# Kernel optimization log

Measured on AMD Instinct MI355X. Metric: run time of the kernel, lower is better.

The kernel has to match this reference:

```python
import jax, jax.numpy as jnp
import numpy as np

COMMITMENT_COST = 0.25
B, T, D = 32, 2048, 64
K = 1024


def setup_inputs() -> dict:
    key = jax.random.key(0)
    k1, k2 = jax.random.split(key)
    inputs = jax.random.normal(k1, (B, T, D), dtype=jnp.float32)
    # codebook init: uniform(-1/K, 1/K) in the original; use same scale
    embedding = jax.random.uniform(k2, (K, D), dtype=jnp.float32,
                                   minval=-1.0 / K, maxval=1.0 / K)
    return {"inputs": inputs, "embedding": embedding}


def reference(inputs, embedding):
    Bb, Tt, Dd = inputs.shape
    flat = inputs.reshape(-1, Dd)  # [N, D]
    dist = (jnp.sum(flat * flat, axis=1, keepdims=True)
            + jnp.sum(embedding * embedding, axis=1)[None, :]
            - 2.0 * (flat @ embedding.T))
    encoding_indices = jnp.argmin(dist, axis=1)  # [N]
    quantized = embedding[encoding_indices].reshape(Bb, Tt, Dd)
    # commitment loss: mse(stop_grad(quantized), inputs)
    e_latent_loss = jnp.mean((jax.lax.stop_gradient(quantized) - inputs) ** 2)
    vq_loss = COMMITMENT_COST * e_latent_loss
    codebook_loss = jnp.zeros((), dtype=jnp.float32)
    # straight-through estimator
    quantized_st = inputs + jax.lax.stop_gradient(quantized - inputs)
    return (quantized_st, encoding_indices.reshape(Bb, Tt),
            vq_loss, e_latent_loss, codebook_loss)
```

## Files before the change

### kernel.cpp

```cpp
#include <hip/hip_runtime.h>
#include <hip/hip_bf16.h>
#include <math.h>


typedef __attribute__((ext_vector_type(8))) short bf16x8;
typedef __attribute__((ext_vector_type(4))) float f32x4;

namespace {
constexpr int NROWS  = 65536;
constexpr int DDIM   = 64;
constexpr int KCODES = 1024;
constexpr float EPSB = 4e-5f;

constexpr size_t WS_LOSS = 0;
constexpr size_t WS_CNT  = 64;
constexpr size_t WS_SE   = 256;
constexpr size_t WS_EHB  = 8192;
constexpr size_t WS_ELB  = WS_EHB + (size_t)65536 * 2;
constexpr size_t WS_BIDX = WS_ELB + (size_t)65536 * 2;
constexpr size_t WS_LIST = WS_BIDX + (size_t)NROWS * 4;
constexpr size_t WS_KEY  = WS_LIST + (size_t)NROWS * 4;
constexpr size_t WS_MV   = WS_KEY + (size_t)NROWS * 8;
constexpr size_t WS_KV   = WS_MV + (size_t)4 * NROWS * 8;
}

__device__ inline short f2bf(float v) {
  __hip_bfloat16 h = __float2bfloat16(v);
  return *reinterpret_cast<short*>(&h);
}
__device__ inline float bf2f(short s) {
  __hip_bfloat16 h;
  *reinterpret_cast<short*>(&h) = s;
  return __bfloat162float(h);
}
__device__ inline f32x4 mfma16(bf16x8 a, bf16x8 b, f32x4 c) {
  return __builtin_amdgcn_mfma_f32_16x16x32_bf16(a, b, c, 0, 0, 0);
}
__device__ inline unsigned int fflip(unsigned int b) {
  return b ^ ((unsigned int)((int)b >> 31) | 0x80000000u);
}

__global__ __launch_bounds__(256) void vq_prep(const float* __restrict__ emb,
                                               float* __restrict__ se,
                                               short* __restrict__ ehB,
                                               short* __restrict__ elB,
                                               unsigned long long* __restrict__ keyBest,
                                               double* __restrict__ loss_accum,
                                               int* __restrict__ cnt) {
  #pragma clang fp contract(off)
  const int gid = blockIdx.x * 256 + (int)threadIdx.x;
  if (gid == 0) { *loss_accum = 0.0; *cnt = 0; }
  keyBest[gid] = ~0ull;

  if (gid < KCODES) {
    const float* e = emb + (size_t)gid * DDIM;
    float r[8];
    #pragma unroll
    for (int j = 0; j < 8; ++j) r[j] = e[j] * e[j];
    #pragma unroll
    for (int i = 8; i < DDIM; i += 8) {
      #pragma unroll
      for (int j = 0; j < 8; ++j) r[j] += e[i + j] * e[i + j];
    }
    se[gid] = ((r[0] + r[1]) + (r[2] + r[3])) + ((r[4] + r[5]) + (r[6] + r[7]));
  }

  if (gid < 8192) {
    const int t  = gid >> 7;
    const int dc = (gid >> 6) & 1;
    const int l  = gid & 63;
    const int code = t * 16 + (l & 15);
    const int d0   = dc * 32 + (l >> 4) * 8;
    const float* ep = emb + (size_t)code * DDIM + d0;
    const size_t ob = ((size_t)(t * 2 + dc) * 64 + l) * 8;
    #pragma unroll
    for (int i = 0; i < 8; ++i) {
      const float v = ep[i];
      const short h = f2bf(v);
      ehB[ob + i] = h;
      elB[ob + i] = f2bf(v - bf2f(h));
    }
  }
}

__global__ __launch_bounds__(256, 2) void vq_fused(const float* __restrict__ x,
                                                   const short* __restrict__ ehB,
                                                   const short* __restrict__ elB,
                                                   const float* __restrict__ se,
                                                   float2* __restrict__ mv,
                                                   unsigned long long* __restrict__ kv) {
  #pragma clang fp contract(off)
  __shared__ float sel[256];
  const int tid  = (int)threadIdx.x;
  const int l    = tid & 63;
  const int wid  = tid >> 6;
  const int quar = (int)blockIdx.x & 3;
  const int rblk = (int)blockIdx.x >> 2;
  const int t0   = quar * 16;
  sel[tid] = se[t0 * 16 + tid];
  __syncthreads();

  const int wrb = rblk * 128 + wid * 32;
  bf16x8 xh[2][2], xl[2][2];
  #pragma unroll
  for (int rt = 0; rt < 2; ++rt) {
    const float* xp = x + (size_t)(wrb + rt * 16 + (l & 15)) * DDIM + (l >> 4) * 8;
    #pragma unroll
    for (int dc = 0; dc < 2; ++dc) {
      const float4 v0 = *reinterpret_cast<const float4*>(xp + dc * 32);
      const float4 v1 = *reinterpret_cast<const float4*>(xp + dc * 32 + 4);
      const float vv[8] = {v0.x, v0.y, v0.z, v0.w, v1.x, v1.y, v1.z, v1.w};
      #pragma unroll
      for (int i = 0; i < 8; ++i) {
        const short h = f2bf(vv[i]);
        xh[rt][dc][i] = h;
        xl[rt][dc][i] = f2bf(vv[i] - bf2f(h));
      }
    }
  }

  float m1v[2][4], m2v[2][4];
  int   m1t[2][4];
  #pragma unroll
  for (int rt = 0; rt < 2; ++rt)
    #pragma unroll
    for (int r = 0; r < 4; ++r) { m1v[rt][r] = INFINITY; m2v[rt][r] = INFINITY; m1t[rt][r] = 0; }

  const size_t lb = (size_t)l * 8;
#define FRAGLD(buf, tt, half2) \
  (*reinterpret_cast<const bf16x8*>((buf) + (size_t)(tt) * 1024 + (half2) * 512 + lb))

  bf16x8 c0 = FRAGLD(ehB, t0, 0), c1 = FRAGLD(ehB, t0, 1),
         c2 = FRAGLD(elB, t0, 0), c3 = FRAGLD(elB, t0, 1);
  bf16x8 n0 = FRAGLD(ehB, t0 + 1, 0), n1 = FRAGLD(ehB, t0 + 1, 1),
         n2 = FRAGLD(elB, t0 + 1, 0), n3 = FRAGLD(elB, t0 + 1, 1);

  const f32x4 kz = {0.f, 0.f, 0.f, 0.f};
  #pragma unroll 4
  for (int tt = 0; tt < 16; ++tt) {
    const int t = t0 + tt;
    const int tf = (tt + 2 < 16) ? t + 2 : t0 + 15;
    bf16x8 f0 = FRAGLD(ehB, tf, 0), f1 = FRAGLD(ehB, tf, 1),
           f2 = FRAGLD(elB, tf, 0), f3 = FRAGLD(elB, tf, 1);

    f32x4 a0, a1;
    a0 = mfma16(xh[0][0], c0, kz);  a1 = mfma16(xh[1][0], c0, kz);
    a0 = mfma16(xh[0][1], c1, a0);  a1 = mfma16(xh[1][1], c1, a1);
    a0 = mfma16(xh[0][0], c2, a0);  a1 = mfma16(xh[1][0], c2, a1);
    a0 = mfma16(xh[0][1], c3, a0);  a1 = mfma16(xh[1][1], c3, a1);
    a0 = mfma16(xl[0][0], c0, a0);  a1 = mfma16(xl[1][0], c0, a1);
    a0 = mfma16(xl[0][1], c1, a0);  a1 = mfma16(xl[1][1], c1, a1);

    const float sev = sel[tt * 16 + (l & 15)];
    #pragma unroll
    for (int r = 0; r < 4; ++r) {
      {
        const float d = __builtin_fmaf(-2.0f, a0[r], sev);
        const bool c = d < m1v[0][r];
        m2v[0][r] = fminf(m2v[0][r], fmaxf(m1v[0][r], d));
        m1t[0][r] = c ? t : m1t[0][r];
        m1v[0][r] = fminf(m1v[0][r], d);
      }
      {
        const float d = __builtin_fmaf(-2.0f, a1[r], sev);
        const bool c = d < m1v[1][r];
        m2v[1][r] = fminf(m2v[1][r], fmaxf(m1v[1][r], d));
        m1t[1][r] = c ? t : m1t[1][r];
        m1v[1][r] = fminf(m1v[1][r], d);
      }
    }
    c0 = n0; c1 = n1; c2 = n2; c3 = n3;
    n0 = f0; n1 = f1; n2 = f2; n3 = f3;
  }
#undef FRAGLD

  const int colbase = l & 15;
  #pragma unroll
  for (int rt = 0; rt < 2; ++rt) {
    #pragma unroll
    for (int r = 0; r < 4; ++r) {
      float m1 = m1v[rt][r], m2 = m2v[rt][r];
      unsigned long long key =
          ((unsigned long long)fflip(__float_as_uint(m1)) << 32)
          | (unsigned)(m1t[rt][r] * 16 + colbase);
      #pragma unroll
      for (int off = 1; off < 16; off <<= 1) {
        const unsigned long long ok = __shfl_xor(key, off, 16);
        const float om1 = __shfl_xor(m1, off, 16);
        const float om2 = __shfl_xor(m2, off, 16);
        m2 = fminf(fminf(m2, om2), fmaxf(m1, om1));
        m1 = fminf(m1, om1);
        key = (ok < key) ? ok : key;
      }
      if (colbase == 0) {
        const int row = wrb + rt * 16 + (l >> 4) * 4 + r;
        mv[(size_t)quar * NROWS + row] = make_float2(m1, m2);
        kv[(size_t)quar * NROWS + row] = key;
      }
    }
  }
}

__global__ __launch_bounds__(256) void vq_combine(const float2* __restrict__ mv,
                                                  const unsigned long long* __restrict__ kv,
                                                  int* __restrict__ bidx,
                                                  int* __restrict__ list,
                                                  int* __restrict__ cnt) {
  const int gid = blockIdx.x * 256 + (int)threadIdx.x;
  const int l = (int)threadIdx.x & 63;
  const float2 A = mv[gid];
  const float2 B = mv[(size_t)NROWS + gid];
  const float2 C = mv[(size_t)2 * NROWS + gid];
  const float2 D = mv[(size_t)3 * NROWS + gid];
  unsigned long long kg = kv[gid];
  {
    unsigned long long k2 = kv[(size_t)NROWS + gid];     kg = (k2 < kg) ? k2 : kg;
    k2 = kv[(size_t)2 * NROWS + gid];                    kg = (k2 < kg) ? k2 : kg;
    k2 = kv[(size_t)3 * NROWS + gid];                    kg = (k2 < kg) ? k2 : kg;
  }
  const float lo1 = fminf(A.x, B.x), hi1 = fmaxf(A.x, B.x);
  const float lo2 = fminf(C.x, D.x), hi2 = fmaxf(C.x, D.x);
  const float m1g = fminf(lo1, lo2);
  const float sec = fminf(fmaxf(lo1, lo2), fminf(hi1, hi2));
  const float m2g = fminf(sec, fminf(fminf(A.y, B.y), fminf(C.y, D.y)));
  const bool cert = m2g > m1g + EPSB;
  bidx[gid] = cert ? (int)(kg & 0xffffffffull) : -1;

  const unsigned long long mask = __ballot(!cert);
  int base = 0;
  if (l == 0 && mask) base = atomicAdd(cnt, (int)__popcll(mask));
  base = __shfl(base, 0, 64);
  if (!cert) {
    const int off = (int)__popcll(mask & ((1ull << l) - 1ull));
    list[base + off] = gid;
  }
}

__global__ __launch_bounds__(64) void vq_exact(const float* __restrict__ x,
                                               const float* __restrict__ emb,
                                               const float* __restrict__ se,
                                               const int* __restrict__ list,
                                               const int* __restrict__ cnt,
                                               unsigned long long* __restrict__ keyBest) {
  #pragma clang fp contract(off)
  __shared__ __align__(16) float eL[32 * DDIM];
  const int n = *cnt;
  if (n == 0) return;
  const int nrb = (n + 63) >> 6;
  const int ntasks = nrb * 32;
  const int l = (int)threadIdx.x;

  for (int t = (int)blockIdx.x; t < ntasks; t += (int)gridDim.x) {
    const int part = t & 31;
    const int rb   = t >> 5;
    const int j0   = part * 32;

    {
      const float4* src = reinterpret_cast<const float4*>(emb + (size_t)j0 * DDIM);
      float4* dst = reinterpret_cast<float4*>(eL);
      #pragma unroll
      for (int i = 0; i < 8; ++i) dst[i * 64 + l] = src[i * 64 + l];
    }
    __syncthreads();

    const int idx = rb * 64 + l;
    const bool act = idx < n;
    const int row = act ? list[idx] : 0;
    const float4* xr4 = reinterpret_cast<const float4*>(x + (size_t)row * DDIM);

    float xv[DDIM];
    #pragma unroll
    for (int q = 0; q < 16; ++q) {
      const float4 v = xr4[q];
      xv[q * 4 + 0] = v.x; xv[q * 4 + 1] = v.y;
      xv[q * 4 + 2] = v.z; xv[q * 4 + 3] = v.w;
    }

    float rr[8];
    #pragma unroll
    for (int j = 0; j < 8; ++j) rr[j] = xv[j] * xv[j];
    #pragma unroll
    for (int i = 8; i < DDIM; i += 8) {
      #pragma unroll
      for (int j = 0; j < 8; ++j) rr[j] += xv[i + j] * xv[i + j];
    }
    const float sx = ((rr[0] + rr[1]) + (rr[2] + rr[3])) + ((rr[4] + rr[5]) + (rr[6] + rr[7]));

    unsigned long long best = ~0ull;
    #pragma unroll 1
    for (int g = 0; g < 8; ++g) {
      const int jb = g * 4;
      const float4* e0 = reinterpret_cast<const float4*>(eL + (jb + 0) * DDIM);
      const float4* e1 = reinterpret_cast<const float4*>(eL + (jb + 1) * DDIM);
      const float4* e2 = reinterpret_cast<const float4*>(eL + (jb + 2) * DDIM);
      const float4* e3 = reinterpret_cast<const float4*>(eL + (jb + 3) * DDIM);
      float a0 = 0.f, a1 = 0.f, a2 = 0.f, a3 = 0.f;
      #pragma unroll
      for (int q = 0; q < 16; ++q) {
        const float4 v0 = e0[q], v1 = e1[q], v2 = e2[q], v3 = e3[q];
        const float xa = xv[q * 4 + 0], xb = xv[q * 4 + 1];
        const float xc = xv[q * 4 + 2], xd = xv[q * 4 + 3];
        a0 = __builtin_fmaf(xa, v0.x, a0); a0 = __builtin_fmaf(xb, v0.y, a0);
        a0 = __builtin_fmaf(xc, v0.z, a0); a0 = __builtin_fmaf(xd, v0.w, a0);
        a1 = __builtin_fmaf(xa, v1.x, a1); a1 = __builtin_fmaf(xb, v1.y, a1);
        a1 = __builtin_fmaf(xc, v1.z, a1); a1 = __builtin_fmaf(xd, v1.w, a1);
        a2 = __builtin_fmaf(xa, v2.x, a2); a2 = __builtin_fmaf(xb, v2.y, a2);
        a2 = __builtin_fmaf(xc, v2.z, a2); a2 = __builtin_fmaf(xd, v2.w, a2);
        a3 = __builtin_fmaf(xa, v3.x, a3); a3 = __builtin_fmaf(xb, v3.y, a3);
        a3 = __builtin_fmaf(xc, v3.z, a3); a3 = __builtin_fmaf(xd, v3.w, a3);
      }
      const int j = j0 + jb;
      const float T0 = sx + se[j + 0];
      const float T1 = sx + se[j + 1];
      const float T2 = sx + se[j + 2];
      const float T3 = sx + se[j + 3];
      const float di0 = __builtin_fmaf(-2.0f, a0, T0);
      const float di1 = __builtin_fmaf(-2.0f, a1, T1);
      const float di2 = __builtin_fmaf(-2.0f, a2, T2);
      const float di3 = __builtin_fmaf(-2.0f, a3, T3);
      unsigned long long k;
      k = ((unsigned long long)fflip(__float_as_uint(di0)) << 32) | (unsigned)(j + 0);
      best = (k < best) ? k : best;
      k = ((unsigned long long)fflip(__float_as_uint(di1)) << 32) | (unsigned)(j + 1);
      best = (k < best) ? k : best;
      k = ((unsigned long long)fflip(__float_as_uint(di2)) << 32) | (unsigned)(j + 2);
      best = (k < best) ? k : best;
      k = ((unsigned long long)fflip(__float_as_uint(di3)) << 32) | (unsigned)(j + 3);
      best = (k < best) ? k : best;
    }
    if (act) atomicMin(&keyBest[row], best);
    __syncthreads();
  }
}

__global__ __launch_bounds__(256) void vq_finalize(const float* __restrict__ x,
                                                   const float* __restrict__ emb,
                                                   const int* __restrict__ bidx,
                                                   const unsigned long long* __restrict__ keyBest,
                                                   float* __restrict__ out,
                                                   double* __restrict__ loss_accum) {
  #pragma clang fp contract(off)
  __shared__ float wsum[4];
  const int tid = (int)threadIdx.x;
  const int l   = tid & 63;
  const int wid = tid >> 6;
  const int sub = l >> 4;
  const int q16 = l & 15;
  float lacc = 0.f;

  #pragma unroll
  for (int it = 0; it < 4; ++it) {
    const int row = blockIdx.x * 64 + it * 16 + wid * 4 + sub;
    int bi = bidx[row];
    if (bi < 0) bi = (int)(keyBest[row] & 0xffffffffull);
    const float4 xv = reinterpret_cast<const float4*>(x)[(size_t)row * 16 + q16];
    const float4 ev = reinterpret_cast<const float4*>(emb)[(size_t)bi * 16 + q16];
    const float da = ev.x - xv.x;
    const float db = ev.y - xv.y;
    const float dc = ev.z - xv.z;
    const float dd = ev.w - xv.w;
    float4 o;
    o.x = xv.x + da; o.y = xv.y + db; o.z = xv.z + dc; o.w = xv.w + dd;
    reinterpret_cast<float4*>(out)[(size_t)row * 16 + q16] = o;
    lacc += da * da + db * db + dc * dc + dd * dd;
    if (q16 == 0) out[(size_t)NROWS * DDIM + row] = (float)bi;
  }
  #pragma unroll
  for (int off = 32; off > 0; off >>= 1) lacc += __shfl_down(lacc, off, 64);
  if (l == 0) wsum[wid] = lacc;
  __syncthreads();
  if (tid == 0)
    atomicAdd(loss_accum, (double)(wsum[0] + wsum[1] + wsum[2] + wsum[3]));
}

__global__ void vq_scalars(const double* __restrict__ loss_accum,
                           float* __restrict__ out) {
  if (threadIdx.x == 0 && blockIdx.x == 0) {
    const double mm = *loss_accum / (double)((size_t)NROWS * DDIM);
    const float el = (float)mm;
    float* tail = out + (size_t)NROWS * DDIM + NROWS;
    tail[0] = 0.25f * el;
    tail[1] = el;
    tail[2] = 0.0f;
  }
}

extern "C" void kernel_launch(void* const* d_in, const int* in_sizes, int n_in,
                              void* d_out, int out_size, void* d_ws, size_t ws_size,
                              hipStream_t stream) {
  const float* x   = (const float*)d_in[0];
  const float* emb = (const float*)d_in[1];
  float* out = (float*)d_out;
  char* ws = (char*)d_ws;

  double* loss_accum = (double*)(ws + WS_LOSS);
  int*    cnt        = (int*)(ws + WS_CNT);
  float*  se         = (float*)(ws + WS_SE);
  short*  ehB        = (short*)(ws + WS_EHB);
  short*  elB        = (short*)(ws + WS_ELB);
  int*    bidx       = (int*)(ws + WS_BIDX);
  int*    list       = (int*)(ws + WS_LIST);
  unsigned long long* keyBest = (unsigned long long*)(ws + WS_KEY);
  float2* mv         = (float2*)(ws + WS_MV);
  unsigned long long* kv = (unsigned long long*)(ws + WS_KV);

  vq_prep<<<NROWS / 256, 256, 0, stream>>>(emb, se, ehB, elB, keyBest,
                                           loss_accum, cnt);
  vq_fused<<<(NROWS / 128) * 4, 256, 0, stream>>>(x, ehB, elB, se, mv, kv);
  vq_combine<<<NROWS / 256, 256, 0, stream>>>(mv, kv, bidx, list, cnt);
  vq_exact<<<2048, 64, 0, stream>>>(x, emb, se, list, cnt, keyBest);
  vq_finalize<<<NROWS / 64, 256, 0, stream>>>(x, emb, bidx, keyBest, out,
                                              loss_accum);
  vq_scalars<<<1, 64, 0, stream>>>(loss_accum, out);
}
```

Before: 98.73 us.

## Double rows per wave in fused VQ kernel and shrink prep launch

```diff
diff --git a/kernel.cpp b/kernel.cpp
--- a/kernel.cpp
+++ b/kernel.cpp
@@ -44,13 +44,11 @@
                                                float* __restrict__ se,
                                                short* __restrict__ ehB,
                                                short* __restrict__ elB,
-                                               unsigned long long* __restrict__ keyBest,
                                                double* __restrict__ loss_accum,
                                                int* __restrict__ cnt) {
   #pragma clang fp contract(off)
   const int gid = blockIdx.x * 256 + (int)threadIdx.x;
   if (gid == 0) { *loss_accum = 0.0; *cnt = 0; }
-  keyBest[gid] = ~0ull;
 
   if (gid < KCODES) {
     const float* e = emb + (size_t)gid * DDIM;
@@ -65,7 +63,7 @@
     se[gid] = ((r[0] + r[1]) + (r[2] + r[3])) + ((r[4] + r[5]) + (r[6] + r[7]));
   }
 
-  if (gid < 8192) {
+  {
     const int t  = gid >> 7;
     const int dc = (gid >> 6) & 1;
     const int l  = gid & 63;
@@ -100,10 +98,10 @@
   sel[tid] = se[t0 * 16 + tid];
   __syncthreads();
 
-  const int wrb = rblk * 128 + wid * 32;
-  bf16x8 xh[2][2], xl[2][2];
+  const int wrb = rblk * 256 + wid * 64;
+  bf16x8 xh[4][2], xl[4][2];
   #pragma unroll
-  for (int rt = 0; rt < 2; ++rt) {
+  for (int rt = 0; rt < 4; ++rt) {
     const float* xp = x + (size_t)(wrb + rt * 16 + (l & 15)) * DDIM + (l >> 4) * 8;
     #pragma unroll
     for (int dc = 0; dc < 2; ++dc) {
@@ -119,10 +117,10 @@
     }
   }
 
-  float m1v[2][4], m2v[2][4];
-  int   m1t[2][4];
+  float m1v[4][4], m2v[4][4];
+  int   m1t[4][4];
   #pragma unroll
-  for (int rt = 0; rt < 2; ++rt)
+  for (int rt = 0; rt < 4; ++rt)
     #pragma unroll
     for (int r = 0; r < 4; ++r) { m1v[rt][r] = INFINITY; m2v[rt][r] = INFINITY; m1t[rt][r] = 0; }
 
@@ -132,51 +130,56 @@
 
   bf16x8 c0 = FRAGLD(ehB, t0, 0), c1 = FRAGLD(ehB, t0, 1),
          c2 = FRAGLD(elB, t0, 0), c3 = FRAGLD(elB, t0, 1);
-  bf16x8 n0 = FRAGLD(ehB, t0 + 1, 0), n1 = FRAGLD(ehB, t0 + 1, 1),
-         n2 = FRAGLD(elB, t0 + 1, 0), n3 = FRAGLD(elB, t0 + 1, 1);
 
   const f32x4 kz = {0.f, 0.f, 0.f, 0.f};
   #pragma unroll 4
   for (int tt = 0; tt < 16; ++tt) {
     const int t = t0 + tt;
-    const int tf = (tt + 2 < 16) ? t + 2 : t0 + 15;
-    bf16x8 f0 = FRAGLD(ehB, tf, 0), f1 = FRAGLD(ehB, tf, 1),
-           f2 = FRAGLD(elB, tf, 0), f3 = FRAGLD(elB, tf, 1);
-
-    f32x4 a0, a1;
+    const int tf = (tt + 1 < 16) ? t + 1 : t;
+    bf16x8 n0 = FRAGLD(ehB, tf, 0), n1 = FRAGLD(ehB, tf, 1),
+           n2 = FRAGLD(elB, tf, 0), n3 = FRAGLD(elB, tf, 1);
+
+    f32x4 a0, a1, a2, a3;
     a0 = mfma16(xh[0][0], c0, kz);  a1 = mfma16(xh[1][0], c0, kz);
+    a2 = mfma16(xh[2][0], c0, kz);  a3 = mfma16(xh[3][0], c0, kz);
     a0 = mfma16(xh[0][1], c1, a0);  a1 = mfma16(xh[1][1], c1, a1);
+    a2 = mfma16(xh[2][1], c1, a2);  a3 = mfma16(xh[3][1], c1, a3);
     a0 = mfma16(xh[0][0], c2, a0);  a1 = mfma16(xh[1][0], c2, a1);
+    a2 = mfma16(xh[2][0], c2, a2);  a3 = mfma16(xh[3][0], c2, a3);
     a0 = mfma16(xh[0][1], c3, a0);  a1 = mfma16(xh[1][1], c3, a1);
+    a2 = mfma16(xh[2][1], c3, a2);  a3 = mfma16(xh[3][1], c3, a3);
     a0 = mfma16(xl[0][0], c0, a0);  a1 = mfma16(xl[1][0], c0, a1);
+    a2 = mfma16(xl[2][0], c0, a2);  a3 = mfma16(xl[3][0], c0, a3);
     a0 = mfma16(xl[0][1], c1, a0);  a1 = mfma16(xl[1][1], c1, a1);
+    a2 = mfma16(xl[2][1], c1, a2);  a3 = mfma16(xl[3][1], c1, a3);
 
     const float sev = sel[tt * 16 + (l & 15)];
     #pragma unroll
     for (int r = 0; r < 4; ++r) {
-      {
-        const float d = __builtin_fmaf(-2.0f, a0[r], sev);
-        const bool c = d < m1v[0][r];
-        m2v[0][r] = fminf(m2v[0][r], fmaxf(m1v[0][r], d));
-        m1t[0][r] = c ? t : m1t[0][r];
-        m1v[0][r] = fminf(m1v[0][r], d);
-      }
-      {
-        const float d = __builtin_fmaf(-2.0f, a1[r], sev);
-        const bool c = d < m1v[1][r];
-        m2v[1][r] = fminf(m2v[1][r], fmaxf(m1v[1][r], d));
-        m1t[1][r] = c ? t : m1t[1][r];
-        m1v[1][r] = fminf(m1v[1][r], d);
-      }
+      const float d0 = __builtin_fmaf(-2.0f, a0[r], sev);
+      const float d1 = __builtin_fmaf(-2.0f, a1[r], sev);
+      const float d2 = __builtin_fmaf(-2.0f, a2[r], sev);
+      const float d3 = __builtin_fmaf(-2.0f, a3[r], sev);
+      m2v[0][r] = __builtin_amdgcn_fmed3f(m1v[0][r], m2v[0][r], d0);
+      m1t[0][r] = (d0 < m1v[0][r]) ? t : m1t[0][r];
+      m1v[0][r] = fminf(m1v[0][r], d0);
+      m2v[1][r] = __builtin_amdgcn_fmed3f(m1v[1][r], m2v[1][r], d1);
+      m1t[1][r] = (d1 < m1v[1][r]) ? t : m1t[1][r];
+      m1v[1][r] = fminf(m1v[1][r], d1);
+      m2v[2][r] = __builtin_amdgcn_fmed3f(m1v[2][r], m2v[2][r], d2);
+      m1t[2][r] = (d2 < m1v[2][r]) ? t : m1t[2][r];
+      m1v[2][r] = fminf(m1v[2][r], d2);
+      m2v[3][r] = __builtin_amdgcn_fmed3f(m1v[3][r], m2v[3][r], d3);
+      m1t[3][r] = (d3 < m1v[3][r]) ? t : m1t[3][r];
+      m1v[3][r] = fminf(m1v[3][r], d3);
     }
     c0 = n0; c1 = n1; c2 = n2; c3 = n3;
-    n0 = f0; n1 = f1; n2 = f2; n3 = f3;
   }
 #undef FRAGLD
 
   const int colbase = l & 15;
   #pragma unroll
-  for (int rt = 0; rt < 2; ++rt) {
+  for (int rt = 0; rt < 4; ++rt) {
     #pragma unroll
     for (int r = 0; r < 4; ++r) {
       float m1 = m1v[rt][r], m2 = m2v[rt][r];
@@ -205,9 +208,11 @@
                                                   const unsigned long long* __restrict__ kv,
                                                   int* __restrict__ bidx,
                                                   int* __restrict__ list,
-                                                  int* __restrict__ cnt) {
+                                                  int* __restrict__ cnt,
+                                                  unsigned long long* __restrict__ keyBest) {
   const int gid = blockIdx.x * 256 + (int)threadIdx.x;
   const int l = (int)threadIdx.x & 63;
+  keyBest[gid] = ~0ull;
   const float2 A = mv[gid];
   const float2 B = mv[(size_t)NROWS + gid];
   const float2 C = mv[(size_t)2 * NROWS + gid];
@@ -404,10 +409,9 @@
   float2* mv         = (float2*)(ws + WS_MV);
   unsigned long long* kv = (unsigned long long*)(ws + WS_KV);
 
-  vq_prep<<<NROWS / 256, 256, 0, stream>>>(emb, se, ehB, elB, keyBest,
-                                           loss_accum, cnt);
-  vq_fused<<<(NROWS / 128) * 4, 256, 0, stream>>>(x, ehB, elB, se, mv, kv);
-  vq_combine<<<NROWS / 256, 256, 0, stream>>>(mv, kv, bidx, list, cnt);
+  vq_prep<<<32, 256, 0, stream>>>(emb, se, ehB, elB, loss_accum, cnt);
+  vq_fused<<<(NROWS / 256) * 4, 256, 0, stream>>>(x, ehB, elB, se, mv, kv);
+  vq_combine<<<NROWS / 256, 256, 0, stream>>>(mv, kv, bidx, list, cnt, keyBest);
   vq_exact<<<2048, 64, 0, stream>>>(x, emb, se, list, cnt, keyBest);
   vq_finalize<<<NROWS / 64, 256, 0, stream>>>(x, emb, bidx, keyBest, out,
                                               loss_accum);
```

After: 105.3 us. 1.07x slower.

## Track top-3 distances to rescore ambiguous rows with two candidates only

Applied to the files above, without the earlier changes.

```diff
diff --git a/kernel.cpp b/kernel.cpp
--- a/kernel.cpp
+++ b/kernel.cpp
@@ -5,6 +5,7 @@
 
 typedef __attribute__((ext_vector_type(8))) short bf16x8;
 typedef __attribute__((ext_vector_type(4))) float f32x4;
+typedef unsigned long long u64;
 
 namespace {
 constexpr int NROWS  = 65536;
@@ -12,16 +13,21 @@
 constexpr int KCODES = 1024;
 constexpr float EPSB = 4e-5f;
 
-constexpr size_t WS_LOSS = 0;
-constexpr size_t WS_CNT  = 64;
-constexpr size_t WS_SE   = 256;
-constexpr size_t WS_EHB  = 8192;
-constexpr size_t WS_ELB  = WS_EHB + (size_t)65536 * 2;
-constexpr size_t WS_BIDX = WS_ELB + (size_t)65536 * 2;
-constexpr size_t WS_LIST = WS_BIDX + (size_t)NROWS * 4;
-constexpr size_t WS_KEY  = WS_LIST + (size_t)NROWS * 4;
-constexpr size_t WS_MV   = WS_KEY + (size_t)NROWS * 8;
-constexpr size_t WS_KV   = WS_MV + (size_t)4 * NROWS * 8;
+constexpr size_t WS_LOSS  = 0;
+constexpr size_t WS_CNT   = 64;
+constexpr size_t WS_CNT2  = 68;
+constexpr size_t WS_DONE  = 72;
+constexpr size_t WS_SE    = 256;
+constexpr size_t WS_EHB   = 8192;
+constexpr size_t WS_ELB   = WS_EHB  + (size_t)65536 * 2;
+constexpr size_t WS_BIDX  = WS_ELB  + (size_t)65536 * 2;
+constexpr size_t WS_LIST  = WS_BIDX + (size_t)NROWS * 4;
+constexpr size_t WS_ROWS2 = WS_LIST + (size_t)NROWS * 4;
+constexpr size_t WS_JJ2   = WS_ROWS2 + (size_t)NROWS * 4;
+constexpr size_t WS_KEY   = WS_JJ2  + (size_t)NROWS * 4;
+constexpr size_t WS_KV1   = WS_KEY  + (size_t)NROWS * 8;
+constexpr size_t WS_KV2   = WS_KV1  + (size_t)4 * NROWS * 8;
+constexpr size_t WS_F3    = WS_KV2  + (size_t)4 * NROWS * 8;
 }
 
 __device__ inline short f2bf(float v) {
@@ -39,18 +45,35 @@
 __device__ inline unsigned int fflip(unsigned int b) {
   return b ^ ((unsigned int)((int)b >> 31) | 0x80000000u);
 }
+__device__ inline float kval(u64 k) {
+  unsigned u = (unsigned)(k >> 32);
+  u ^= ((int)u < 0) ? 0x80000000u : 0xFFFFFFFFu;
+  return __uint_as_float(u);
+}
+
+struct Tri { u64 k1, k2; float f1, f2, f3; };
+__device__ inline Tri tmerge(const Tri& A, const Tri& B) {
+  const bool aw = A.k1 <= B.k1;
+  const u64  w2k = aw ? A.k2 : B.k2, l1k = aw ? B.k1 : A.k1;
+  const float w2f = aw ? A.f2 : B.f2, l1f = aw ? B.f1 : A.f1;
+  const float w3f = aw ? A.f3 : B.f3, l2f = aw ? B.f2 : A.f2;
+  Tri r;
+  r.k1 = aw ? A.k1 : B.k1;  r.f1 = aw ? A.f1 : B.f1;
+  const bool s = w2k <= l1k;
+  r.k2 = s ? w2k : l1k;     r.f2 = s ? w2f : l1f;
+  r.f3 = fminf(fmaxf(w2f, l1f), fminf(w3f, l2f));
+  return r;
+}
 
 __global__ __launch_bounds__(256) void vq_prep(const float* __restrict__ emb,
                                                float* __restrict__ se,
                                                short* __restrict__ ehB,
                                                short* __restrict__ elB,
-                                               unsigned long long* __restrict__ keyBest,
                                                double* __restrict__ loss_accum,
-                                               int* __restrict__ cnt) {
+                                               int* __restrict__ cnts) {
   #pragma clang fp contract(off)
   const int gid = blockIdx.x * 256 + (int)threadIdx.x;
-  if (gid == 0) { *loss_accum = 0.0; *cnt = 0; }
-  keyBest[gid] = ~0ull;
+  if (gid == 0) { *loss_accum = 0.0; cnts[0] = 0; cnts[1] = 0; cnts[2] = 0; }
 
   if (gid < KCODES) {
     const float* e = emb + (size_t)gid * DDIM;
@@ -65,7 +88,7 @@
     se[gid] = ((r[0] + r[1]) + (r[2] + r[3])) + ((r[4] + r[5]) + (r[6] + r[7]));
   }
 
-  if (gid < 8192) {
+  {
     const int t  = gid >> 7;
     const int dc = (gid >> 6) & 1;
     const int l  = gid & 63;
@@ -87,8 +110,9 @@
                                                    const short* __restrict__ ehB,
                                                    const short* __restrict__ elB,
                                                    const float* __restrict__ se,
-                                                   float2* __restrict__ mv,
-                                                   unsigned long long* __restrict__ kv) {
+                                                   u64* __restrict__ kv1,
+                                                   u64* __restrict__ kv2,
+                                                   float* __restrict__ f3v) {
   #pragma clang fp contract(off)
   __shared__ float sel[256];
   const int tid  = (int)threadIdx.x;
@@ -119,12 +143,15 @@
     }
   }
 
-  float m1v[2][4], m2v[2][4];
-  int   m1t[2][4];
+  float m1v[2][4], m2v[2][4], m3v[2][4];
+  int   m1t[2][4], m2t[2][4];
   #pragma unroll
   for (int rt = 0; rt < 2; ++rt)
     #pragma unroll
-    for (int r = 0; r < 4; ++r) { m1v[rt][r] = INFINITY; m2v[rt][r] = INFINITY; m1t[rt][r] = 0; }
+    for (int r = 0; r < 4; ++r) {
+      m1v[rt][r] = INFINITY; m2v[rt][r] = INFINITY; m3v[rt][r] = INFINITY;
+      m1t[rt][r] = 0; m2t[rt][r] = 0;
+    }
 
   const size_t lb = (size_t)l * 8;
 #define FRAGLD(buf, tt, half2) \
@@ -156,16 +183,22 @@
     for (int r = 0; r < 4; ++r) {
       {
         const float d = __builtin_fmaf(-2.0f, a0[r], sev);
-        const bool c = d < m1v[0][r];
-        m2v[0][r] = fminf(m2v[0][r], fmaxf(m1v[0][r], d));
-        m1t[0][r] = c ? t : m1t[0][r];
+        const bool lt1 = d < m1v[0][r];
+        const bool lt2 = d < m2v[0][r];
+        m3v[0][r] = __builtin_amdgcn_fmed3f(m2v[0][r], m3v[0][r], d);
+        m2t[0][r] = lt1 ? m1t[0][r] : (lt2 ? t : m2t[0][r]);
+        m2v[0][r] = __builtin_amdgcn_fmed3f(m1v[0][r], m2v[0][r], d);
+        m1t[0][r] = lt1 ? t : m1t[0][r];
         m1v[0][r] = fminf(m1v[0][r], d);
       }
       {
         const float d = __builtin_fmaf(-2.0f, a1[r], sev);
-        const bool c = d < m1v[1][r];
-        m2v[1][r] = fminf(m2v[1][r], fmaxf(m1v[1][r], d));
-        m1t[1][r] = c ? t : m1t[1][r];
+        const bool lt1 = d < m1v[1][r];
+        const bool lt2 = d < m2v[1][r];
+        m3v[1][r] = __builtin_amdgcn_fmed3f(m2v[1][r], m3v[1][r], d);
+        m2t[1][r] = lt1 ? m1t[1][r] : (lt2 ? t : m2t[1][r]);
+        m2v[1][r] = __builtin_amdgcn_fmed3f(m1v[1][r], m2v[1][r], d);
+        m1t[1][r] = lt1 ? t : m1t[1][r];
         m1v[1][r] = fminf(m1v[1][r], d);
       }
     }
@@ -179,60 +212,136 @@
   for (int rt = 0; rt < 2; ++rt) {
     #pragma unroll
     for (int r = 0; r < 4; ++r) {
-      float m1 = m1v[rt][r], m2 = m2v[rt][r];
-      unsigned long long key =
-          ((unsigned long long)fflip(__float_as_uint(m1)) << 32)
-          | (unsigned)(m1t[rt][r] * 16 + colbase);
+      Tri T;
+      T.k1 = ((u64)fflip(__float_as_uint(m1v[rt][r])) << 32)
+             | (unsigned)(m1t[rt][r] * 16 + colbase);
+      T.k2 = ((u64)fflip(__float_as_uint(m2v[rt][r])) << 32)
+             | (unsigned)(m2t[rt][r] * 16 + colbase);
+      T.f1 = m1v[rt][r]; T.f2 = m2v[rt][r]; T.f3 = m3v[rt][r];
       #pragma unroll
       for (int off = 1; off < 16; off <<= 1) {
-        const unsigned long long ok = __shfl_xor(key, off, 16);
-        const float om1 = __shfl_xor(m1, off, 16);
-        const float om2 = __shfl_xor(m2, off, 16);
-        m2 = fminf(fminf(m2, om2), fmaxf(m1, om1));
-        m1 = fminf(m1, om1);
-        key = (ok < key) ? ok : key;
+        Tri O;
+        O.k1 = __shfl_xor(T.k1, off, 16);
+        O.k2 = __shfl_xor(T.k2, off, 16);
+        O.f1 = __shfl_xor(T.f1, off, 16);
+        O.f2 = __shfl_xor(T.f2, off, 16);
+        O.f3 = __shfl_xor(T.f3, off, 16);
+        T = tmerge(T, O);
       }
       if (colbase == 0) {
         const int row = wrb + rt * 16 + (l >> 4) * 4 + r;
-        mv[(size_t)quar * NROWS + row] = make_float2(m1, m2);
-        kv[(size_t)quar * NROWS + row] = key;
+        kv1[(size_t)quar * NROWS + row] = T.k1;
+        kv2[(size_t)quar * NROWS + row] = T.k2;
+        f3v[(size_t)quar * NROWS + row] = T.f3;
       }
     }
   }
 }
 
-__global__ __launch_bounds__(256) void vq_combine(const float2* __restrict__ mv,
-                                                  const unsigned long long* __restrict__ kv,
+__global__ __launch_bounds__(256) void vq_combine(const u64* __restrict__ kv1,
+                                                  const u64* __restrict__ kv2,
+                                                  const float* __restrict__ f3v,
                                                   int* __restrict__ bidx,
                                                   int* __restrict__ list,
-                                                  int* __restrict__ cnt) {
+                                                  int* __restrict__ rows2,
+                                                  int* __restrict__ jj2,
+                                                  int* __restrict__ cnts,
+                                                  u64* __restrict__ keyBest) {
   const int gid = blockIdx.x * 256 + (int)threadIdx.x;
   const int l = (int)threadIdx.x & 63;
-  const float2 A = mv[gid];
-  const float2 B = mv[(size_t)NROWS + gid];
-  const float2 C = mv[(size_t)2 * NROWS + gid];
-  const float2 D = mv[(size_t)3 * NROWS + gid];
-  unsigned long long kg = kv[gid];
+  keyBest[gid] = ~0ull;
+
+  Tri Q[4];
+  #pragma unroll
+  for (int q = 0; q < 4; ++q) {
+    Q[q].k1 = kv1[(size_t)q * NROWS + gid];
+    Q[q].k2 = kv2[(size_t)q * NROWS + gid];
+    Q[q].f1 = kval(Q[q].k1);
+    Q[q].f2 = kval(Q[q].k2);
+    Q[q].f3 = f3v[(size_t)q * NROWS + gid];
+  }
+  const Tri Z = tmerge(tmerge(Q[0], Q[1]), tmerge(Q[2], Q[3]));
+
+  const bool cert  = Z.f2 > Z.f1 + EPSB;
+  const bool two   = !cert && (Z.f3 > Z.f1 + EPSB);
+  const bool full  = !cert && !two;
+
+  bidx[gid] = cert ? (int)(Z.k1 & 0xffffffffull) : -1;
+
   {
-    unsigned long long k2 = kv[(size_t)NROWS + gid];     kg = (k2 < kg) ? k2 : kg;
-    k2 = kv[(size_t)2 * NROWS + gid];                    kg = (k2 < kg) ? k2 : kg;
-    k2 = kv[(size_t)3 * NROWS + gid];                    kg = (k2 < kg) ? k2 : kg;
-  }
-  const float lo1 = fminf(A.x, B.x), hi1 = fmaxf(A.x, B.x);
-  const float lo2 = fminf(C.x, D.x), hi2 = fmaxf(C.x, D.x);
-  const float m1g = fminf(lo1, lo2);
-  const float sec = fminf(fmaxf(lo1, lo2), fminf(hi1, hi2));
-  const float m2g = fminf(sec, fminf(fminf(A.y, B.y), fminf(C.y, D.y)));
-  const bool cert = m2g > m1g + EPSB;
-  bidx[gid] = cert ? (int)(kg & 0xffffffffull) : -1;
-
-  const unsigned long long mask = __ballot(!cert);
-  int base = 0;
-  if (l == 0 && mask) base = atomicAdd(cnt, (int)__popcll(mask));
-  base = __shfl(base, 0, 64);
-  if (!cert) {
-    const int off = (int)__popcll(mask & ((1ull << l) - 1ull));
-    list[base + off] = gid;
+    const u64 mask = __ballot(two);
+    int base = 0;
+    if (l == 0 && mask) base = atomicAdd(&cnts[1], (int)__popcll(mask));
+    base = __shfl(base, 0, 64);
+    if (two) {
+      const int off = (int)__popcll(mask & ((1ull << l) - 1ull));
+      rows2[base + off] = gid;
+      jj2[base + off] = ((int)(Z.k1 & 0xffffull) << 16) | (int)(Z.k2 & 0xffffull);
+    }
+  }
+  {
+    const u64 mask = __ballot(full);
+    int base = 0;
+    if (l == 0 && mask) base = atomicAdd(&cnts[0], (int)__popcll(mask));
+    base = __shfl(base, 0, 64);
+    if (full) {
+      const int off = (int)__popcll(mask & ((1ull << l) - 1ull));
+      list[base + off] = gid;
+    }
+  }
+}
+
+__global__ __launch_bounds__(256) void vq_rescore2(const float* __restrict__ x,
+                                                   const float* __restrict__ emb,
+                                                   const float* __restrict__ se,
+                                                   const int* __restrict__ rows2,
+                                                   const int* __restrict__ jj2,
+                                                   const int* __restrict__ cnts,
+                                                   int* __restrict__ bidx) {
+  #pragma clang fp contract(off)
+  const int n2 = cnts[1];
+  for (int idx = blockIdx.x * 256 + (int)threadIdx.x; idx < n2;
+       idx += (int)gridDim.x * 256) {
+    const int row = rows2[idx];
+    const int jj  = jj2[idx];
+    const int j1  = jj >> 16;
+    const int j2  = jj & 0xffff;
+    const float4* xr4 = reinterpret_cast<const float4*>(x + (size_t)row * DDIM);
+    const float4* e14 = reinterpret_cast<const float4*>(emb + (size_t)j1 * DDIM);
+    const float4* e24 = reinterpret_cast<const float4*>(emb + (size_t)j2 * DDIM);
+
+    float rr[8];
+    {
+      const float4 a = xr4[0], b = xr4[1];
+      rr[0] = a.x * a.x; rr[1] = a.y * a.y; rr[2] = a.z * a.z; rr[3] = a.w * a.w;
+      rr[4] = b.x * b.x; rr[5] = b.y * b.y; rr[6] = b.z * b.z; rr[7] = b.w * b.w;
+    }
+    #pragma unroll
+    for (int i = 2; i < 16; i += 2) {
+      const float4 a = xr4[i], b = xr4[i + 1];
+      rr[0] += a.x * a.x; rr[1] += a.y * a.y; rr[2] += a.z * a.z; rr[3] += a.w * a.w;
+      rr[4] += b.x * b.x; rr[5] += b.y * b.y; rr[6] += b.z * b.z; rr[7] += b.w * b.w;
+    }
+    const float sx = ((rr[0] + rr[1]) + (rr[2] + rr[3])) + ((rr[4] + rr[5]) + (rr[6] + rr[7]));
+
+    float a1 = 0.f, a2 = 0.f;
+    #pragma unroll
+    for (int q = 0; q < 16; ++q) {
+      const float4 xv = xr4[q];
+      const float4 v1 = e14[q];
+      const float4 v2 = e24[q];
+      a1 = __builtin_fmaf(xv.x, v1.x, a1); a1 = __builtin_fmaf(xv.y, v1.y, a1);
+      a1 = __builtin_fmaf(xv.z, v1.z, a1); a1 = __builtin_fmaf(xv.w, v1.w, a1);
+      a2 = __builtin_fmaf(xv.x, v2.x, a2); a2 = __builtin_fmaf(xv.y, v2.y, a2);
+      a2 = __builtin_fmaf(xv.z, v2.z, a2); a2 = __builtin_fmaf(xv.w, v2.w, a2);
+    }
+    const float T1 = sx + se[j1];
+    const float T2 = sx + se[j2];
+    const float D1 = __builtin_fmaf(-2.0f, a1, T1);
+    const float D2 = __builtin_fmaf(-2.0f, a2, T2);
+    const u64 k1 = ((u64)fflip(__float_as_uint(D1)) << 32) | (unsigned)j1;
+    const u64 k2 = ((u64)fflip(__float_as_uint(D2)) << 32) | (unsigned)j2;
+    bidx[row] = (int)(((k1 < k2) ? k1 : k2) & 0xffffffffull);
   }
 }
 
@@ -240,11 +349,11 @@
                                                const float* __restrict__ emb,
                                                const float* __restrict__ se,
                                                const int* __restrict__ list,
-                                               const int* __restrict__ cnt,
-                                               unsigned long long* __restrict__ keyBest) {
+                                               const int* __restrict__ cnts,
+                                               u64* __restrict__ keyBest) {
   #pragma clang fp contract(off)
   __shared__ __align__(16) float eL[32 * DDIM];
-  const int n = *cnt;
+  const int n = cnts[0];
   if (n == 0) return;
   const int nrb = (n + 63) >> 6;
   const int ntasks = nrb * 32;
@@ -286,7 +395,7 @@
     }
     const float sx = ((rr[0] + rr[1]) + (rr[2] + rr[3])) + ((rr[4] + rr[5]) + (rr[6] + rr[7]));
 
-    unsigned long long best = ~0ull;
+    u64 best = ~0ull;
     #pragma unroll 1
     for (int g = 0; g < 8; ++g) {
       const int jb = g * 4;
@@ -318,14 +427,14 @@
       const float di1 = __builtin_fmaf(-2.0f, a1, T1);
       const float di2 = __builtin_fmaf(-2.0f, a2, T2);
       const float di3 = __builtin_fmaf(-2.0f, a3, T3);
-      unsigned long long k;
-      k = ((unsigned long long)fflip(__float_as_uint(di0)) << 32) | (unsigned)(j + 0);
+      u64 k;
+      k = ((u64)fflip(__float_as_uint(di0)) << 32) | (unsigned)(j + 0);
       best = (k < best) ? k : best;
-      k = ((unsigned long long)fflip(__float_as_uint(di1)) << 32) | (unsigned)(j + 1);
+      k = ((u64)fflip(__float_as_uint(di1)) << 32) | (unsigned)(j + 1);
       best = (k < best) ? k : best;
-      k = ((unsigned long long)fflip(__float_as_uint(di2)) << 32) | (unsigned)(j + 2);
+      k = ((u64)fflip(__float_as_uint(di2)) << 32) | (unsigned)(j + 2);
       best = (k < best) ? k : best;
-      k = ((unsigned long long)fflip(__float_as_uint(di3)) << 32) | (unsigned)(j + 3);
+      k = ((u64)fflip(__float_as_uint(di3)) << 32) | (unsigned)(j + 3);
       best = (k < best) ? k : best;
     }
     if (act) atomicMin(&keyBest[row], best);
@@ -336,9 +445,10 @@
 __global__ __launch_bounds__(256) void vq_finalize(const float* __restrict__ x,
                                                    const float* __restrict__ emb,
                                                    const int* __restrict__ bidx,
-                                                   const unsigned long long* __restrict__ keyBest,
+                                                   const u64* __restrict__ keyBest,
                                                    float* __restrict__ out,
-                                                   double* __restrict__ loss_accum) {
+                                                   double* __restrict__ loss_accum,
+                                                   int* __restrict__ done) {
   #pragma clang fp contract(off)
   __shared__ float wsum[4];
   const int tid = (int)threadIdx.x;
@@ -369,19 +479,18 @@
   for (int off = 32; off > 0; off >>= 1) lacc += __shfl_down(lacc, off, 64);
   if (l == 0) wsum[wid] = lacc;
   __syncthreads();
-  if (tid == 0)
+  if (tid == 0) {
     atomicAdd(loss_accum, (double)(wsum[0] + wsum[1] + wsum[2] + wsum[3]));
-}
-
-__global__ void vq_scalars(const double* __restrict__ loss_accum,
-                           float* __restrict__ out) {
-  if (threadIdx.x == 0 && blockIdx.x == 0) {
-    const double mm = *loss_accum / (double)((size_t)NROWS * DDIM);
-    const float el = (float)mm;
-    float* tail = out + (size_t)NROWS * DDIM + NROWS;
-    tail[0] = 0.25f * el;
-    tail[1] = el;
-    tail[2] = 0.0f;
+    __threadfence();
+    if (atomicAdd(done, 1) == (int)gridDim.x - 1) {
+      __threadfence();
+      const double mm = *loss_accum / (double)((size_t)NROWS * DDIM);
+      const float el = (float)mm;
+      float* tail = out + (size_t)NROWS * DDIM + NROWS;
+      tail[0] = 0.25f * el;
+      tail[1] = el;
+      tail[2] = 0.0f;
+    }
   }
 }
 
@@ -394,22 +503,26 @@
   char* ws = (char*)d_ws;
 
   double* loss_accum = (double*)(ws + WS_LOSS);
-  int*    cnt        = (int*)(ws + WS_CNT);
+  int*    cnts       = (int*)(ws + WS_CNT);
+  int*    done       = (int*)(ws + WS_DONE);
   float*  se         = (float*)(ws + WS_SE);
   short*  ehB        = (short*)(ws + WS_EHB);
   short*  elB        = (short*)(ws + WS_ELB);
   int*    bidx       = (int*)(ws + WS_BIDX);
   int*    list       = (int*)(ws + WS_LIST);
-  unsigned long long* keyBest = (unsigned long long*)(ws + WS_KEY);
-  float2* mv         = (float2*)(ws + WS_MV);
-  unsigned long long* kv = (unsigned long long*)(ws + WS_KV);
-
-  vq_prep<<<NROWS / 256, 256, 0, stream>>>(emb, se, ehB, elB, keyBest,
-                                           loss_accum, cnt);
-  vq_fused<<<(NROWS / 128) * 4, 256, 0, stream>>>(x, ehB, elB, se, mv, kv);
-  vq_combine<<<NROWS / 256, 256, 0, stream>>>(mv, kv, bidx, list, cnt);
-  vq_exact<<<2048, 64, 0, stream>>>(x, emb, se, list, cnt, keyBest);
+  int*    rows2      = (int*)(ws + WS_ROWS2);
+  int*    jj2        = (int*)(ws + WS_JJ2);
+  u64*    keyBest    = (u64*)(ws + WS_KEY);
+  u64*    kv1        = (u64*)(ws + WS_KV1);
+  u64*    kv2        = (u64*)(ws + WS_KV2);
+  float*  f3v        = (float*)(ws + WS_F3);
+
+  vq_prep<<<32, 256, 0, stream>>>(emb, se, ehB, elB, loss_accum, cnts);
+  vq_fused<<<(NROWS / 128) * 4, 256, 0, stream>>>(x, ehB, elB, se, kv1, kv2, f3v);
+  vq_combine<<<NROWS / 256, 256, 0, stream>>>(kv1, kv2, f3v, bidx, list,
+                                              rows2, jj2, cnts, keyBest);
+  vq_rescore2<<<256, 256, 0, stream>>>(x, emb, se, rows2, jj2, cnts, bidx);
+  vq_exact<<<2048, 64, 0, stream>>>(x, emb, se, list, cnts, keyBest);
   vq_finalize<<<NROWS / 64, 256, 0, stream>>>(x, emb, bidx, keyBest, out,
-                                              loss_accum);
-  vq_scalars<<<1, 64, 0, stream>>>(loss_accum, out);
-}
+                                              loss_accum, done);
+}
```

After: 146.6 us. +48.5%, slower.

## Fold scalar tail into finalize, move keyBest init, split MFMA chains

Applied to the files above, without the earlier changes.

```diff
diff --git a/kernel.cpp b/kernel.cpp
--- a/kernel.cpp
+++ b/kernel.cpp
@@ -5,6 +5,7 @@
 
 typedef __attribute__((ext_vector_type(8))) short bf16x8;
 typedef __attribute__((ext_vector_type(4))) float f32x4;
+typedef unsigned long long u64;
 
 namespace {
 constexpr int NROWS  = 65536;
@@ -44,13 +45,11 @@
                                                float* __restrict__ se,
                                                short* __restrict__ ehB,
                                                short* __restrict__ elB,
-                                               unsigned long long* __restrict__ keyBest,
                                                double* __restrict__ loss_accum,
-                                               int* __restrict__ cnt) {
+                                               int* __restrict__ cnts) {
   #pragma clang fp contract(off)
   const int gid = blockIdx.x * 256 + (int)threadIdx.x;
-  if (gid == 0) { *loss_accum = 0.0; *cnt = 0; }
-  keyBest[gid] = ~0ull;
+  if (gid == 0) { *loss_accum = 0.0; cnts[0] = 0; cnts[1] = 0; }
 
   if (gid < KCODES) {
     const float* e = emb + (size_t)gid * DDIM;
@@ -65,7 +64,7 @@
     se[gid] = ((r[0] + r[1]) + (r[2] + r[3])) + ((r[4] + r[5]) + (r[6] + r[7]));
   }
 
-  if (gid < 8192) {
+  {
     const int t  = gid >> 7;
     const int dc = (gid >> 6) & 1;
     const int l  = gid & 63;
@@ -88,7 +87,7 @@
                                                    const short* __restrict__ elB,
                                                    const float* __restrict__ se,
                                                    float2* __restrict__ mv,
-                                                   unsigned long long* __restrict__ kv) {
+                                                   u64* __restrict__ kv) {
   #pragma clang fp contract(off)
   __shared__ float sel[256];
   const int tid  = (int)threadIdx.x;
@@ -143,29 +142,29 @@
     bf16x8 f0 = FRAGLD(ehB, tf, 0), f1 = FRAGLD(ehB, tf, 1),
            f2 = FRAGLD(elB, tf, 0), f3 = FRAGLD(elB, tf, 1);
 
-    f32x4 a0, a1;
+    f32x4 a0, a1, b0, b1;
     a0 = mfma16(xh[0][0], c0, kz);  a1 = mfma16(xh[1][0], c0, kz);
-    a0 = mfma16(xh[0][1], c1, a0);  a1 = mfma16(xh[1][1], c1, a1);
+    b0 = mfma16(xh[0][1], c1, kz);  b1 = mfma16(xh[1][1], c1, kz);
     a0 = mfma16(xh[0][0], c2, a0);  a1 = mfma16(xh[1][0], c2, a1);
-    a0 = mfma16(xh[0][1], c3, a0);  a1 = mfma16(xh[1][1], c3, a1);
+    b0 = mfma16(xh[0][1], c3, b0);  b1 = mfma16(xh[1][1], c3, b1);
     a0 = mfma16(xl[0][0], c0, a0);  a1 = mfma16(xl[1][0], c0, a1);
-    a0 = mfma16(xl[0][1], c1, a0);  a1 = mfma16(xl[1][1], c1, a1);
+    b0 = mfma16(xl[0][1], c1, b0);  b1 = mfma16(xl[1][1], c1, b1);
 
     const float sev = sel[tt * 16 + (l & 15)];
     #pragma unroll
     for (int r = 0; r < 4; ++r) {
       {
-        const float d = __builtin_fmaf(-2.0f, a0[r], sev);
-        const bool c = d < m1v[0][r];
-        m2v[0][r] = fminf(m2v[0][r], fmaxf(m1v[0][r], d));
-        m1t[0][r] = c ? t : m1t[0][r];
+        const float s = a0[r] + b0[r];
+        const float d = __builtin_fmaf(-2.0f, s, sev);
+        m2v[0][r] = __builtin_amdgcn_fmed3f(m1v[0][r], m2v[0][r], d);
+        m1t[0][r] = (d < m1v[0][r]) ? t : m1t[0][r];
         m1v[0][r] = fminf(m1v[0][r], d);
       }
       {
-        const float d = __builtin_fmaf(-2.0f, a1[r], sev);
-        const bool c = d < m1v[1][r];
-        m2v[1][r] = fminf(m2v[1][r], fmaxf(m1v[1][r], d));
-        m1t[1][r] = c ? t : m1t[1][r];
+        const float s = a1[r] + b1[r];
+        const float d = __builtin_fmaf(-2.0f, s, sev);
+        m2v[1][r] = __builtin_amdgcn_fmed3f(m1v[1][r], m2v[1][r], d);
+        m1t[1][r] = (d < m1v[1][r]) ? t : m1t[1][r];
         m1v[1][r] = fminf(m1v[1][r], d);
       }
     }
@@ -180,12 +179,11 @@
     #pragma unroll
     for (int r = 0; r < 4; ++r) {
       float m1 = m1v[rt][r], m2 = m2v[rt][r];
-      unsigned long long key =
-          ((unsigned long long)fflip(__float_as_uint(m1)) << 32)
-          | (unsigned)(m1t[rt][r] * 16 + colbase);
+      u64 key = ((u64)fflip(__float_as_uint(m1)) << 32)
+                | (unsigned)(m1t[rt][r] * 16 + colbase);
       #pragma unroll
       for (int off = 1; off < 16; off <<= 1) {
-        const unsigned long long ok = __shfl_xor(key, off, 16);
+        const u64 ok = __shfl_xor(key, off, 16);
         const float om1 = __shfl_xor(m1, off, 16);
         const float om2 = __shfl_xor(m2, off, 16);
         m2 = fminf(fminf(m2, om2), fmaxf(m1, om1));
@@ -202,21 +200,23 @@
 }
 
 __global__ __launch_bounds__(256) void vq_combine(const float2* __restrict__ mv,
-                                                  const unsigned long long* __restrict__ kv,
+                                                  const u64* __restrict__ kv,
                                                   int* __restrict__ bidx,
                                                   int* __restrict__ list,
-                                                  int* __restrict__ cnt) {
+                                                  int* __restrict__ cnts,
+                                                  u64* __restrict__ keyBest) {
   const int gid = blockIdx.x * 256 + (int)threadIdx.x;
   const int l = (int)threadIdx.x & 63;
+  keyBest[gid] = ~0ull;
   const float2 A = mv[gid];
   const float2 B = mv[(size_t)NROWS + gid];
   const float2 C = mv[(size_t)2 * NROWS + gid];
   const float2 D = mv[(size_t)3 * NROWS + gid];
-  unsigned long long kg = kv[gid];
+  u64 kg = kv[gid];
   {
-    unsigned long long k2 = kv[(size_t)NROWS + gid];     kg = (k2 < kg) ? k2 : kg;
-    k2 = kv[(size_t)2 * NROWS + gid];                    kg = (k2 < kg) ? k2 : kg;
-    k2 = kv[(size_t)3 * NROWS + gid];                    kg = (k2 < kg) ? k2 : kg;
+    u64 k2 = kv[(size_t)NROWS + gid];     kg = (k2 < kg) ? k2 : kg;
+    k2 = kv[(size_t)2 * NROWS + gid];     kg = (k2 < kg) ? k2 : kg;
+    k2 = kv[(size_t)3 * NROWS + gid];     kg = (k2 < kg) ? k2 : kg;
   }
   const float lo1 = fminf(A.x, B.x), hi1 = fmaxf(A.x, B.x);
   const float lo2 = fminf(C.x, D.x), hi2 = fmaxf(C.x, D.x);
@@ -226,9 +226,9 @@
   const bool cert = m2g > m1g + EPSB;
   bidx[gid] = cert ? (int)(kg & 0xffffffffull) : -1;
 
-  const unsigned long long mask = __ballot(!cert);
+  const u64 mask = __ballot(!cert);
   int base = 0;
-  if (l == 0 && mask) base = atomicAdd(cnt, (int)__popcll(mask));
+  if (l == 0 && mask) base = atomicAdd(&cnts[0], (int)__popcll(mask));
   base = __shfl(base, 0, 64);
   if (!cert) {
     const int off = (int)__popcll(mask & ((1ull << l) - 1ull));
@@ -240,11 +240,11 @@
                                                const float* __restrict__ emb,
                                                const float* __restrict__ se,
                                                const int* __restrict__ list,
-                                               const int* __restrict__ cnt,
-                                               unsigned long long* __restrict__ keyBest) {
+                                               const int* __restrict__ cnts,
+                                               u64* __restrict__ keyBest) {
   #pragma clang fp contract(off)
   __shared__ __align__(16) float eL[32 * DDIM];
-  const int n = *cnt;
+  const int n = cnts[0];
   if (n == 0) return;
   const int nrb = (n + 63) >> 6;
   const int ntasks = nrb * 32;
@@ -286,7 +286,7 @@
     }
     const float sx = ((rr[0] + rr[1]) + (rr[2] + rr[3])) + ((rr[4] + rr[5]) + (rr[6] + rr[7]));
 
-    unsigned long long best = ~0ull;
+    u64 best = ~0ull;
     #pragma unroll 1
     for (int g = 0; g < 8; ++g) {
       const int jb = g * 4;
@@ -318,14 +318,14 @@
       const float di1 = __builtin_fmaf(-2.0f, a1, T1);
       const float di2 = __builtin_fmaf(-2.0f, a2, T2);
       const float di3 = __builtin_fmaf(-2.0f, a3, T3);
-      unsigned long long k;
-      k = ((unsigned long long)fflip(__float_as_uint(di0)) << 32) | (unsigned)(j + 0);
+      u64 k;
+      k = ((u64)fflip(__float_as_uint(di0)) << 32) | (unsigned)(j + 0);
       best = (k < best) ? k : best;
-      k = ((unsigned long long)fflip(__float_as_uint(di1)) << 32) | (unsigned)(j + 1);
+      k = ((u64)fflip(__float_as_uint(di1)) << 32) | (unsigned)(j + 1);
       best = (k < best) ? k : best;
-      k = ((unsigned long long)fflip(__float_as_uint(di2)) << 32) | (unsigned)(j + 2);
+      k = ((u64)fflip(__float_as_uint(di2)) << 32) | (unsigned)(j + 2);
       best = (k < best) ? k : best;
-      k = ((unsigned long long)fflip(__float_as_uint(di3)) << 32) | (unsigned)(j + 3);
+      k = ((u64)fflip(__float_as_uint(di3)) << 32) | (unsigned)(j + 3);
       best = (k < best) ? k : best;
     }
     if (act) atomicMin(&keyBest[row], best);
@@ -336,9 +336,10 @@
 __global__ __launch_bounds__(256) void vq_finalize(const float* __restrict__ x,
                                                    const float* __restrict__ emb,
                                                    const int* __restrict__ bidx,
-                                                   const unsigned long long* __restrict__ keyBest,
+                                                   const u64* __restrict__ keyBest,
                                                    float* __restrict__ out,
-                                                   double* __restrict__ loss_accum) {
+                                                   double* __restrict__ loss_accum,
+                                                   int* __restrict__ cnts) {
   #pragma clang fp contract(off)
   __shared__ float wsum[4];
   const int tid = (int)threadIdx.x;
@@ -369,19 +370,18 @@
   for (int off = 32; off > 0; off >>= 1) lacc += __shfl_down(lacc, off, 64);
   if (l == 0) wsum[wid] = lacc;
   __syncthreads();
-  if (tid == 0)
+  if (tid == 0) {
     atomicAdd(loss_accum, (double)(wsum[0] + wsum[1] + wsum[2] + wsum[3]));
-}
-
-__global__ void vq_scalars(const double* __restrict__ loss_accum,
-                           float* __restrict__ out) {
-  if (threadIdx.x == 0 && blockIdx.x == 0) {
-    const double mm = *loss_accum / (double)((size_t)NROWS * DDIM);
-    const float el = (float)mm;
-    float* tail = out + (size_t)NROWS * DDIM + NROWS;
-    tail[0] = 0.25f * el;
-    tail[1] = el;
-    tail[2] = 0.0f;
+    __threadfence();
+    if (atomicAdd(&cnts[1], 1) == (int)gridDim.x - 1) {
+      __threadfence();
+      const double mm = *loss_accum / (double)((size_t)NROWS * DDIM);
+      const float el = (float)mm;
+      float* tail = out + (size_t)NROWS * DDIM + NROWS;
+      tail[0] = 0.25f * el;
+      tail[1] = el;
+      tail[2] = 0.0f;
+    }
   }
 }
 
@@ -394,22 +394,20 @@
   char* ws = (char*)d_ws;
 
   double* loss_accum = (double*)(ws + WS_LOSS);
-  int*    cnt        = (int*)(ws + WS_CNT);
+  int*    cnts       = (int*)(ws + WS_CNT);
   float*  se         = (float*)(ws + WS_SE);
   short*  ehB        = (short*)(ws + WS_EHB);
   short*  elB        = (short*)(ws + WS_ELB);
   int*    bidx       = (int*)(ws + WS_BIDX);
   int*    list       = (int*)(ws + WS_LIST);
-  unsigned long long* keyBest = (unsigned long long*)(ws + WS_KEY);
+  u64*    keyBest    = (u64*)(ws + WS_KEY);
   float2* mv         = (float2*)(ws + WS_MV);
-  unsigned long long* kv = (unsigned long long*)(ws + WS_KV);
-
-  vq_prep<<<NROWS / 256, 256, 0, stream>>>(emb, se, ehB, elB, keyBest,
-                                           loss_accum, cnt);
+  u64*    kv         = (u64*)(ws + WS_KV);
+
+  vq_prep<<<32, 256, 0, stream>>>(emb, se, ehB, elB, loss_accum, cnts);
   vq_fused<<<(NROWS / 128) * 4, 256, 0, stream>>>(x, ehB, elB, se, mv, kv);
-  vq_combine<<<NROWS / 256, 256, 0, stream>>>(mv, kv, bidx, list, cnt);
-  vq_exact<<<2048, 64, 0, stream>>>(x, emb, se, list, cnt, keyBest);
+  vq_combine<<<NROWS / 256, 256, 0, stream>>>(mv, kv, bidx, list, cnts, keyBest);
+  vq_exact<<<2048, 64, 0, stream>>>(x, emb, se, list, cnts, keyBest);
   vq_finalize<<<NROWS / 64, 256, 0, stream>>>(x, emb, bidx, keyBest, out,
-                                              loss_accum);
-  vq_scalars<<<1, 64, 0, stream>>>(loss_accum, out);
-}
+                                              loss_accum, cnts);
+}
```

Measured after the change: 113.2 us. 14.7% more time.
